# Kernel optimization log

Measured on AMD Instinct MI355X. Metric: run time of the kernel, lower is better.

The kernel has to match this reference:

```python
import jax, jax.numpy as jnp
import numpy as np


def polymatmul(x, d):
    """Matrix multiply of 2x2 matrices whose entries are polynomials.

    x: (b, n, 2, 2, d1)  -- batch of per-diagonal-block 2x2 polynomial matrices
    d: (n, 2, 2, d2)     -- per-block 2x2 polynomial matrices (the diagonal params)
    Returns: (b, n, 2, 2, d1 + d2 - 1)
    out[b,n,i,j,:] = sum_k full_conv(x[b,n,i,k,:], d[n,k,j,:])
    Implemented by looping over the (small) d2 coefficient axis and accumulating
    shifted 2x2 matmuls, so the only large intermediate is the output itself.
    """
    d1 = x.shape[-1]
    d2 = d.shape[-1]
    out = jnp.zeros(x.shape[:-1] + (d1 + d2 - 1,), dtype=x.dtype)
    for v in range(d2):
        # contract over k (the inner 2-dim), broadcast over poly coeff axis u
        term = jnp.einsum('bniku,nkj->bniju', x, d[..., v])
        out = out.at[..., v:v + d1].add(term)
    return out


def setup_inputs() -> dict:
    key = jax.random.key(0)
    k1, k2, k3 = jax.random.split(key, 3)
    size, deg = 8192, 7
    b, d1 = 64, 16
    input_ = jax.random.normal(k1, (b, 2 * size, 2, 2, d1), dtype=jnp.float32)
    diag1 = jax.random.normal(k2, (size, 2, 2, deg + 1), dtype=jnp.float32)
    diag2 = jax.random.normal(k3, (size, 2, 2, deg + 1), dtype=jnp.float32)
    return {"input_": input_, "diag1": diag1, "diag2": diag2}


def reference(input_, diag1, diag2):
    size = diag1.shape[0]
    # HstackDiag.forward: sum of the two polynomial block-diagonal matmuls
    return polymatmul(input_[:, :size], diag1) + polymatmul(input_[:, size:], diag2)
```

## Files before the change

kernel.cpp:

```cpp
#include <hip/hip_runtime.h>
#include <stdint.h>

#define BB 64
#define NN 8192
#define TILE 64
#define DOUT 23
#define TPB 4

__device__ __forceinline__ int swz(int G) { return G ^ ((G >> 3) & 7); }

typedef const __attribute__((address_space(1))) uint32_t* gas_u32p;
typedef __attribute__((address_space(3))) uint32_t* las_u32p;

__device__ __forceinline__ void stage_gll(const float4* __restrict__ gsrc,
                                          float4* dst, int w, int lane) {
#pragma unroll
    for (int r = 0; r < 4; ++r) {
        const int C = (r * 4 + w) * 64 + lane;
        const int S = swz(C);
        __builtin_amdgcn_global_load_lds((gas_u32p)(const void*)(gsrc + S),
                                         (las_u32p)(void*)(dst + (r * 4 + w) * 64),
                                         16, 0, 0);
    }
}

__device__ __forceinline__ void compute_half(const float4* __restrict__ buf,
                                             const float4* __restrict__ dp,
                                             int unit, int i, float* __restrict__ acc) {
#pragma unroll
    for (int k = 0; k < 2; ++k) {
        float4 dq0 = dp[k * 4 + 0], dq1 = dp[k * 4 + 1];
        const float dv[8] = {dq0.x, dq0.y, dq0.z, dq0.w,
                             dq1.x, dq1.y, dq1.z, dq1.w};
#pragma unroll
        for (int q = 0; q < 4; ++q) {
            float4 xq = buf[swz(unit * 16 + i * 8 + k * 4 + q)];
            const float xe[4] = {xq.x, xq.y, xq.z, xq.w};
#pragma unroll
            for (int e = 0; e < 4; ++e) {
#pragma unroll
                for (int v = 0; v < 8; ++v) {
                    acc[q * 4 + e + v] += xe[e] * dv[v];
                }
            }
        }
    }
}

__global__ __launch_bounds__(256) void hstackdiag_kernel(
    const float* __restrict__ input,
    const float* __restrict__ diag1,
    const float* __restrict__ diag2,
    float* __restrict__ out) {
    __shared__ float4 bufA[1024];
    __shared__ float4 bufB[1024];

    const int t = threadIdx.x;
    const int lane = t & 63;
    const int w = t >> 6;
    const int tile0 = blockIdx.x * TPB;
    const int b = tile0 >> 7;
    int n0 = (tile0 & 127) * TILE;

    const int j = t & 1;
    const int i = (t >> 1) & 1;
    const int unit = t >> 2;

    const float4* gbase = (const float4*)input + (size_t)b * (2 * NN) * 16;

    stage_gll(gbase + (size_t)n0 * 16, bufA, w, lane);

    for (int tt = 0; tt < TPB; ++tt) {
        const int n = n0 + unit;
        const float4* dp1 = (const float4*)diag1 + (size_t)n * 8 + j * 2;
        const float4* dp2 = (const float4*)diag2 + (size_t)n * 8 + j * 2;

        __syncthreads();
        stage_gll(gbase + (size_t)(NN + n0) * 16, bufB, w, lane);

        float acc[DOUT];
#pragma unroll
        for (int u = 0; u < DOUT; ++u) acc[u] = 0.0f;

        compute_half(bufA, dp1, unit, i, acc);

        __syncthreads();
        if (tt < TPB - 1)
            stage_gll(gbase + (size_t)(n0 + TILE) * 16, bufA, w, lane);

        compute_half(bufB, dp2, unit, i, acc);

        __syncthreads();

        float* sout = (float*)bufB;
        float4* sout4 = bufB;
        float* gout = out + ((size_t)b * NN + n0) * (4 * DOUT);
        const int c = i * 2 + j;
#pragma unroll
        for (int p = 0; p < 2; ++p) {
            if ((unit >> 5) == p) {
#pragma unroll
                for (int q = 0; q < DOUT; ++q)
                    sout[(unit & 31) * 92 + c * DOUT + q] = acc[q];
            }
            __syncthreads();
            float4* g4 = (float4*)(gout + p * 2944);
#pragma unroll
            for (int rr = 0; rr < 2; ++rr) g4[rr * 256 + t] = sout4[rr * 256 + t];
            if (t < 224) g4[512 + t] = sout4[512 + t];
            if (p == 0) __syncthreads();
        }
        n0 += TILE;
    }
}

extern "C" void kernel_launch(void* const* d_in, const int* in_sizes, int n_in,
                              void* d_out, int out_size, void* d_ws, size_t ws_size,
                              hipStream_t stream) {
    const float* input = (const float*)d_in[0];
    const float* diag1 = (const float*)d_in[1];
    const float* diag2 = (const float*)d_in[2];
    float* out = (float*)d_out;

    const int grid = BB * (NN / TILE) / TPB;
    hstackdiag_kernel<<<grid, 256, 0, stream>>>(input, diag1, diag2, out);
}
```

Measured before the change: 100.8 us.

## Make each wave own a private LDS region and drop block-wide barriers

Each block now handles one 64-block tile, and each wave stages, computes and writes back its own 16 blocks in a private LDS region. This removes every __syncthreads; waves wait only on their own vmcnt. The multi-tile-per-block loop and its double-buffered prefetch are gone, and the grid grows fourfold. The diagonal loads are hoisted into registers, and the swizzle is changed to suit the per-wave layout. In exchange, per-block load/compute overlap is lost, and the kernel relies on wave-level memory ordering for LDS reuse within a wave.

```diff
diff --git a/kernel.cpp b/kernel.cpp
--- a/kernel.cpp
+++ b/kernel.cpp
@@ -3,38 +3,27 @@
 
 #define BB 64
 #define NN 8192
-#define TILE 64
 #define DOUT 23
-#define TPB 4
-
-__device__ __forceinline__ int swz(int G) { return G ^ ((G >> 3) & 7); }
 
 typedef const __attribute__((address_space(1))) uint32_t* gas_u32p;
 typedef __attribute__((address_space(3))) uint32_t* las_u32p;
 
-__device__ __forceinline__ void stage_gll(const float4* __restrict__ gsrc,
-                                          float4* dst, int w, int lane) {
-#pragma unroll
-    for (int r = 0; r < 4; ++r) {
-        const int C = (r * 4 + w) * 64 + lane;
-        const int S = swz(C);
-        __builtin_amdgcn_global_load_lds((gas_u32p)(const void*)(gsrc + S),
-                                         (las_u32p)(void*)(dst + (r * 4 + w) * 64),
-                                         16, 0, 0);
-    }
-}
+__device__ __forceinline__ int swz8(int F) { return F ^ ((F >> 4) & 15); }
 
-__device__ __forceinline__ void compute_half(const float4* __restrict__ buf,
-                                             const float4* __restrict__ dp,
-                                             int unit, int i, float* __restrict__ acc) {
+__device__ __forceinline__ void half_acc(const float4* __restrict__ region,
+                                         int base, int u16, int i,
+                                         float4 k0a, float4 k0b,
+                                         float4 k1a, float4 k1b,
+                                         float* __restrict__ acc) {
 #pragma unroll
     for (int k = 0; k < 2; ++k) {
-        float4 dq0 = dp[k * 4 + 0], dq1 = dp[k * 4 + 1];
-        const float dv[8] = {dq0.x, dq0.y, dq0.z, dq0.w,
-                             dq1.x, dq1.y, dq1.z, dq1.w};
+        const float4 q0 = k ? k1a : k0a;
+        const float4 q1 = k ? k1b : k0b;
+        const float dv[8] = {q0.x, q0.y, q0.z, q0.w, q1.x, q1.y, q1.z, q1.w};
 #pragma unroll
         for (int q = 0; q < 4; ++q) {
-            float4 xq = buf[swz(unit * 16 + i * 8 + k * 4 + q)];
+            const int F = u16 * 16 + i * 8 + k * 4 + q;
+            const float4 xq = region[base + swz8(F)];
             const float xe[4] = {xq.x, xq.y, xq.z, xq.w};
 #pragma unroll
             for (int e = 0; e < 4; ++e) {
@@ -52,66 +41,65 @@
     const float* __restrict__ diag1,
     const float* __restrict__ diag2,
     float* __restrict__ out) {
-    __shared__ float4 bufA[1024];
-    __shared__ float4 bufB[1024];
+    __shared__ float4 lds[2048];
 
     const int t = threadIdx.x;
     const int lane = t & 63;
     const int w = t >> 6;
-    const int tile0 = blockIdx.x * TPB;
-    const int b = tile0 >> 7;
-    int n0 = (tile0 & 127) * TILE;
+    const int bx = blockIdx.x;
+    const int b = bx >> 7;
+    const int n0w = (bx & 127) * 64 + w * 16;
 
-    const int j = t & 1;
-    const int i = (t >> 1) & 1;
-    const int unit = t >> 2;
+    float4* region = lds + w * 512;
 
-    const float4* gbase = (const float4*)input + (size_t)b * (2 * NN) * 16;
+    const float4* gb = (const float4*)input +
+                       (size_t)b * (2 * NN) * 16 + (size_t)n0w * 16;
+    const float4* gb2 = gb + (size_t)NN * 16;
+#pragma unroll
+    for (int r = 0; r < 4; ++r) {
+        const int S = swz8(r * 64 + lane);
+        __builtin_amdgcn_global_load_lds((gas_u32p)(const void*)(gb + S),
+                                         (las_u32p)(void*)(region + r * 64),
+                                         16, 0, 0);
+    }
+#pragma unroll
+    for (int r = 0; r < 4; ++r) {
+        const int S = swz8(r * 64 + lane);
+        __builtin_amdgcn_global_load_lds((gas_u32p)(const void*)(gb2 + S),
+                                         (las_u32p)(void*)(region + 256 + r * 64),
+                                         16, 0, 0);
+    }
 
-    stage_gll(gbase + (size_t)n0 * 16, bufA, w, lane);
+    const int u16 = lane >> 2;
+    const int i = (lane >> 1) & 1;
+    const int j = lane & 1;
+    const int n = n0w + u16;
+    const float4* dp1 = (const float4*)diag1 + (size_t)n * 8 + j * 2;
+    const float4* dp2 = (const float4*)diag2 + (size_t)n * 8 + j * 2;
+    const float4 d1k0a = dp1[0], d1k0b = dp1[1], d1k1a = dp1[4], d1k1b = dp1[5];
+    const float4 d2k0a = dp2[0], d2k0b = dp2[1], d2k1a = dp2[4], d2k1b = dp2[5];
 
-    for (int tt = 0; tt < TPB; ++tt) {
-        const int n = n0 + unit;
-        const float4* dp1 = (const float4*)diag1 + (size_t)n * 8 + j * 2;
-        const float4* dp2 = (const float4*)diag2 + (size_t)n * 8 + j * 2;
+    asm volatile("s_waitcnt vmcnt(0)" ::: "memory");
 
-        __syncthreads();
-        stage_gll(gbase + (size_t)(NN + n0) * 16, bufB, w, lane);
+    float acc[DOUT];
+#pragma unroll
+    for (int u = 0; u < DOUT; ++u) acc[u] = 0.0f;
 
-        float acc[DOUT];
+    half_acc(region, 0, u16, i, d1k0a, d1k0b, d1k1a, d1k1b, acc);
+    half_acc(region, 256, u16, i, d2k0a, d2k0b, d2k1a, d2k1b, acc);
+
+    float* sf = (float*)region;
+    const int c = i * 2 + j;
 #pragma unroll
-        for (int u = 0; u < DOUT; ++u) acc[u] = 0.0f;
-
-        compute_half(bufA, dp1, unit, i, acc);
-
-        __syncthreads();
-        if (tt < TPB - 1)
-            stage_gll(gbase + (size_t)(n0 + TILE) * 16, bufA, w, lane);
-
-        compute_half(bufB, dp2, unit, i, acc);
-
-        __syncthreads();
-
-        float* sout = (float*)bufB;
-        float4* sout4 = bufB;
-        float* gout = out + ((size_t)b * NN + n0) * (4 * DOUT);
-        const int c = i * 2 + j;
+    for (int q = 0; q < DOUT; ++q) {
+        sf[u16 * 92 + c * DOUT + q] = acc[q];
+    }
+    float4* gout = (float4*)(out + ((size_t)b * NN + n0w) * (4 * DOUT));
 #pragma unroll
-        for (int p = 0; p < 2; ++p) {
-            if ((unit >> 5) == p) {
-#pragma unroll
-                for (int q = 0; q < DOUT; ++q)
-                    sout[(unit & 31) * 92 + c * DOUT + q] = acc[q];
-            }
-            __syncthreads();
-            float4* g4 = (float4*)(gout + p * 2944);
-#pragma unroll
-            for (int rr = 0; rr < 2; ++rr) g4[rr * 256 + t] = sout4[rr * 256 + t];
-            if (t < 224) g4[512 + t] = sout4[512 + t];
-            if (p == 0) __syncthreads();
-        }
-        n0 += TILE;
+    for (int m = 0; m < 5; ++m) {
+        gout[m * 64 + lane] = region[m * 64 + lane];
     }
+    if (lane < 48) gout[320 + lane] = region[320 + lane];
 }
 
 extern "C" void kernel_launch(void* const* d_in, const int* in_sizes, int n_in,
@@ -122,6 +110,6 @@
     const float* diag2 = (const float*)d_in[2];
     float* out = (float*)d_out;
 
-    const int grid = BB * (NN / TILE) / TPB;
+    const int grid = BB * (NN / 64);
     hstackdiag_kernel<<<grid, 256, 0, stream>>>(input, diag1, diag2, out);
 }
```

New measurement: 90.78 us. 9.9% less time.
